# Performance work log

Measured on AMD Instinct MI355X. Metric: run time of the kernel, lower is better.

## Reference

```python
import jax, jax.numpy as jnp
import numpy as np

ALPHA = 1.0


def setup_inputs() -> dict:
    key = jax.random.key(0)
    k1, k2 = jax.random.split(key)
    B, T, N, L = 512, 50, 6400, 10
    spikes = jax.random.uniform(k1, (B, T, N), dtype=jnp.float32)
    labels = jax.random.randint(k2, (B,), 0, L, dtype=jnp.int64)
    rates = jnp.zeros((N, L), dtype=jnp.float32)
    return {"spikes": spikes, "labels": labels, "rates": rates, "n_labels": L}


def reference(spikes, labels, rates, n_labels):
    # spikes: [B, T, N]; labels: [B]; rates: [N, L]
    s = spikes.sum(axis=1)  # [B, N] spike counts per sample
    # segment-sum over batch keyed by label (replaces per-label nonzero+gather loop)
    seg_sum = jax.ops.segment_sum(s, labels, num_segments=n_labels)          # [L, N]
    counts = jax.ops.segment_sum(jnp.ones(labels.shape, s.dtype), labels,
                                 num_segments=n_labels)                       # [L]
    mean = seg_sum / jnp.maximum(counts, 1.0)[:, None]                        # [L, N]
    # original only updates column i when that label is present in the batch
    rates_new = jnp.where(counts[None, :] > 0, ALPHA * rates + mean.T, rates)  # [N, L]
    assignments = jnp.argmax(rates_new, axis=1)                               # [N]
    return assignments, rates_new
```

## Files before the change

### kernel.cpp

```cpp
#include <hip/hip_runtime.h>
#include <math.h>


#define L_FIXED 10

__global__ void __launch_bounds__(64) partial2_k(
    const float* __restrict__ spikes, const int* __restrict__ labels,
    float* __restrict__ part, int B, int T, int N, int GB) {
    const int g = blockIdx.y;
    const int v = blockIdx.x * blockDim.x + threadIdx.x;
    const int V = N >> 1;
    if (v >= V) return;

    float a0[L_FIXED], a1[L_FIXED];
#pragma unroll
    for (int l = 0; l < L_FIXED; ++l) { a0[l] = 0.f; a1[l] = 0.f; }

    const int b0 = g * GB;
    const int b1 = (b0 + GB < B) ? (b0 + GB) : B;
    for (int b = b0; b < b1; ++b) {
        const float2* p = (const float2*)(spikes + (size_t)b * T * N) + v;
        float s0 = 0.f, s1 = 0.f;
#pragma unroll 10
        for (int t = 0; t < T; ++t) {
            float2 x = p[(size_t)t * V];
            s0 += x.x; s1 += x.y;
        }
        const int lab = labels[b];
#pragma unroll
        for (int l = 0; l < L_FIXED; ++l)
            if (lab == l) { a0[l] += s0; a1[l] += s1; }
    }

    float* dst = part + (size_t)g * L_FIXED * N;
#pragma unroll
    for (int l = 0; l < L_FIXED; ++l) {
        ((float2*)(dst + (size_t)l * N))[v] = make_float2(a0[l], a1[l]);
    }
}

__global__ void __launch_bounds__(64) partial1_k(
    const float* __restrict__ spikes, const int* __restrict__ labels,
    float* __restrict__ part, int B, int T, int N, int GB) {
    const int g = blockIdx.y;
    const int n = blockIdx.x * blockDim.x + threadIdx.x;
    if (n >= N) return;

    float a[L_FIXED];
#pragma unroll
    for (int l = 0; l < L_FIXED; ++l) a[l] = 0.f;

    const int b0 = g * GB;
    const int b1 = (b0 + GB < B) ? (b0 + GB) : B;
    for (int b = b0; b < b1; ++b) {
        const float* p = spikes + (size_t)b * T * N + n;
        float s = 0.f;
#pragma unroll 10
        for (int t = 0; t < T; ++t) s += p[(size_t)t * N];
        const int lab = labels[b];
#pragma unroll
        for (int l = 0; l < L_FIXED; ++l)
            if (lab == l) a[l] += s;
    }
    float* dst = part + (size_t)g * L_FIXED * N;
#pragma unroll
    for (int l = 0; l < L_FIXED; ++l) dst[(size_t)l * N + n] = a[l];
}

__global__ void __launch_bounds__(256) finalize_k(
    const float* __restrict__ part, const int* __restrict__ labels,
    const float* __restrict__ rates, float* __restrict__ out,
    int B, int N, int NG, float alpha) {
    __shared__ int cnt[L_FIXED];
    if (threadIdx.x < L_FIXED) cnt[threadIdx.x] = 0;
    __syncthreads();
    for (int b = threadIdx.x; b < B; b += blockDim.x)
        atomicAdd(&cnt[labels[b]], 1);
    __syncthreads();

    const int n = blockIdx.x * blockDim.x + threadIdx.x;
    if (n >= N) return;

    float best = -INFINITY;
    int bi = 0;
#pragma unroll
    for (int l = 0; l < L_FIXED; ++l) {
        double s = 0.0;
        for (int g = 0; g < NG; ++g)
            s += (double)part[((size_t)g * L_FIXED + l) * N + n];
        const int c = cnt[l];
        const float r = rates[(size_t)n * L_FIXED + l];
        const float v = (c > 0) ? (alpha * r + (float)(s / (double)c)) : r;
        out[(size_t)N + (size_t)n * L_FIXED + l] = v;
        if (v > best) { best = v; bi = l; }
    }
    out[n] = (float)bi;
}

extern "C" void kernel_launch(void* const* d_in, const int* in_sizes, int n_in,
                              void* d_out, int out_size, void* d_ws, size_t ws_size,
                              hipStream_t stream) {
    const float* spikes = (const float*)d_in[0];
    const int*   labels = (const int*)d_in[1];
    const float* rates  = (const float*)d_in[2];
    const int L = L_FIXED;
    const int B = in_sizes[1];
    const int N = in_sizes[2] / L;
    const int T = in_sizes[0] / (B * N);
    float* out = (float*)d_out;

    const size_t per = (size_t)L * N * sizeof(float);
    int NG = 64;
    if (per > 0 && (size_t)NG * per > ws_size) NG = (int)(ws_size / per);
    if (NG < 1) NG = 1;
    if (NG > B) NG = B;
    const int GB = (B + NG - 1) / NG;
    float* part = (float*)d_ws;

    if ((N & 1) == 0) {
        const int V = N >> 1;
        dim3 g((V + 63) / 64, NG);
        partial2_k<<<g, dim3(64), 0, stream>>>(spikes, labels, part, B, T, N, GB);
    } else {
        dim3 g((N + 63) / 64, NG);
        partial1_k<<<g, dim3(64), 0, stream>>>(spikes, labels, part, B, T, N, GB);
    }

    finalize_k<<<dim3((N + 255) / 256), dim3(256), 0, stream>>>(
        part, labels, rates, out, B, N, NG, 1.0f);
}
```

Baseline: 987.9 us.

## Split time-sum per sample and move label bucketing into a parallel finalize

The first stage now launches one block per (sample, time-half) and sums spikes over time with float4 loads into a per-sample partial buffer, instead of grouping batches per thread with per-label accumulators. The finalize kernel then does the label segment-sum itself, splitting partial rows across 8 wavefronts with labels cached in shared memory, and reduces those in shared memory before applying the rate update and argmax. The aim is higher occupancy and wider contiguous loads in the bandwidth-bound reduction. The cost is a larger intermediate buffer (HS*B*N floats) that finalize must read back, which adds memory traffic.

```diff
diff --git a/kernel.cpp b/kernel.cpp
--- a/kernel.cpp
+++ b/kernel.cpp
@@ -4,98 +4,127 @@
 
 #define L_FIXED 10
 
-__global__ void __launch_bounds__(64) partial2_k(
-    const float* __restrict__ spikes, const int* __restrict__ labels,
-    float* __restrict__ part, int B, int T, int N, int GB) {
-    const int g = blockIdx.y;
-    const int v = blockIdx.x * blockDim.x + threadIdx.x;
-    const int V = N >> 1;
-    if (v >= V) return;
+__global__ void __launch_bounds__(320) sumT_lin_k(
+    const float* __restrict__ spikes, float* __restrict__ part,
+    int B, int T, int N, int HS) {
+    const int r = blockIdx.x;
+    const int h = r / B;
+    const int b = r - h * B;
+    const int t0 = (T * h) / HS;
+    const int t1 = (T * (h + 1)) / HS;
+    const int V = N >> 2;
+    const int tid = threadIdx.x;
+    const float4* p = (const float4*)(spikes + (size_t)b * T * N);
+    float4* dst = (float4*)(part + (size_t)r * N);
 
-    float a0[L_FIXED], a1[L_FIXED];
-#pragma unroll
-    for (int l = 0; l < L_FIXED; ++l) { a0[l] = 0.f; a1[l] = 0.f; }
-
-    const int b0 = g * GB;
-    const int b1 = (b0 + GB < B) ? (b0 + GB) : B;
-    for (int b = b0; b < b1; ++b) {
-        const float2* p = (const float2*)(spikes + (size_t)b * T * N) + v;
-        float s0 = 0.f, s1 = 0.f;
-#pragma unroll 10
-        for (int t = 0; t < T; ++t) {
-            float2 x = p[(size_t)t * V];
-            s0 += x.x; s1 += x.y;
+    for (int v0 = 0; v0 < V; v0 += 1600) {
+        float4 a0 = make_float4(0.f, 0.f, 0.f, 0.f);
+        float4 a1 = a0, a2 = a0, a3 = a0, a4 = a0;
+        const int c0 = v0 + tid;
+#pragma unroll 2
+        for (int t = t0; t < t1; ++t) {
+            const float4* row = p + (size_t)t * V;
+            if (c0 < V)        { float4 x = row[c0];        a0.x += x.x; a0.y += x.y; a0.z += x.z; a0.w += x.w; }
+            if (c0 + 320 < V)  { float4 x = row[c0 + 320];  a1.x += x.x; a1.y += x.y; a1.z += x.z; a1.w += x.w; }
+            if (c0 + 640 < V)  { float4 x = row[c0 + 640];  a2.x += x.x; a2.y += x.y; a2.z += x.z; a2.w += x.w; }
+            if (c0 + 960 < V)  { float4 x = row[c0 + 960];  a3.x += x.x; a3.y += x.y; a3.z += x.z; a3.w += x.w; }
+            if (c0 + 1280 < V) { float4 x = row[c0 + 1280]; a4.x += x.x; a4.y += x.y; a4.z += x.z; a4.w += x.w; }
         }
-        const int lab = labels[b];
-#pragma unroll
-        for (int l = 0; l < L_FIXED; ++l)
-            if (lab == l) { a0[l] += s0; a1[l] += s1; }
-    }
-
-    float* dst = part + (size_t)g * L_FIXED * N;
-#pragma unroll
-    for (int l = 0; l < L_FIXED; ++l) {
-        ((float2*)(dst + (size_t)l * N))[v] = make_float2(a0[l], a1[l]);
+        if (c0 < V)        dst[c0]        = a0;
+        if (c0 + 320 < V)  dst[c0 + 320]  = a1;
+        if (c0 + 640 < V)  dst[c0 + 640]  = a2;
+        if (c0 + 960 < V)  dst[c0 + 960]  = a3;
+        if (c0 + 1280 < V) dst[c0 + 1280] = a4;
     }
 }
 
-__global__ void __launch_bounds__(64) partial1_k(
-    const float* __restrict__ spikes, const int* __restrict__ labels,
-    float* __restrict__ part, int B, int T, int N, int GB) {
-    const int g = blockIdx.y;
+__global__ void __launch_bounds__(256) sumT1h_k(
+    const float* __restrict__ spikes, float* __restrict__ part,
+    int B, int T, int N, int HS) {
+    const int r = blockIdx.y;
+    const int h = r / B;
+    const int b = r - h * B;
+    const int t0 = (T * h) / HS;
+    const int t1 = (T * (h + 1)) / HS;
     const int n = blockIdx.x * blockDim.x + threadIdx.x;
     if (n >= N) return;
-
-    float a[L_FIXED];
-#pragma unroll
-    for (int l = 0; l < L_FIXED; ++l) a[l] = 0.f;
-
-    const int b0 = g * GB;
-    const int b1 = (b0 + GB < B) ? (b0 + GB) : B;
-    for (int b = b0; b < b1; ++b) {
-        const float* p = spikes + (size_t)b * T * N + n;
-        float s = 0.f;
-#pragma unroll 10
-        for (int t = 0; t < T; ++t) s += p[(size_t)t * N];
-        const int lab = labels[b];
-#pragma unroll
-        for (int l = 0; l < L_FIXED; ++l)
-            if (lab == l) a[l] += s;
-    }
-    float* dst = part + (size_t)g * L_FIXED * N;
-#pragma unroll
-    for (int l = 0; l < L_FIXED; ++l) dst[(size_t)l * N + n] = a[l];
+    const float* p = spikes + (size_t)b * T * N + n;
+    float s = 0.f;
+    for (int t = t0; t < t1; ++t) s += p[(size_t)t * N];
+    part[(size_t)r * N + n] = s;
 }
 
-__global__ void __launch_bounds__(256) finalize_k(
+__global__ void __launch_bounds__(512) finalize2_k(
     const float* __restrict__ part, const int* __restrict__ labels,
     const float* __restrict__ rates, float* __restrict__ out,
-    int B, int N, int NG, float alpha) {
+    int B, int N, int NR, float alpha) {
     __shared__ int cnt[L_FIXED];
-    if (threadIdx.x < L_FIXED) cnt[threadIdx.x] = 0;
+    __shared__ short slab[2048];
+    __shared__ double red[8][64][L_FIXED];
+
+    const int tid = threadIdx.x;
+    if (tid < L_FIXED) cnt[tid] = 0;
     __syncthreads();
-    for (int b = threadIdx.x; b < B; b += blockDim.x)
-        atomicAdd(&cnt[labels[b]], 1);
+    const bool use_slab = (NR <= 2048);
+    const int HS = NR / B;
+    for (int i = tid; i < B; i += blockDim.x) {
+        const int lb = labels[i];
+        atomicAdd(&cnt[lb], 1);
+        if (use_slab)
+            for (int h = 0; h < HS; ++h) slab[h * B + i] = (short)lb;
+    }
     __syncthreads();
 
-    const int n = blockIdx.x * blockDim.x + threadIdx.x;
-    if (n >= N) return;
+    const int lane = tid & 63;
+    const int q = tid >> 6;
+    const int n = blockIdx.x * 64 + lane;
 
-    float best = -INFINITY;
-    int bi = 0;
+    double a[L_FIXED];
 #pragma unroll
-    for (int l = 0; l < L_FIXED; ++l) {
-        double s = 0.0;
-        for (int g = 0; g < NG; ++g)
-            s += (double)part[((size_t)g * L_FIXED + l) * N + n];
-        const int c = cnt[l];
-        const float r = rates[(size_t)n * L_FIXED + l];
-        const float v = (c > 0) ? (alpha * r + (float)(s / (double)c)) : r;
-        out[(size_t)N + (size_t)n * L_FIXED + l] = v;
-        if (v > best) { best = v; bi = l; }
+    for (int l = 0; l < L_FIXED; ++l) a[l] = 0.0;
+
+    if (n < N) {
+        if (use_slab) {
+#pragma unroll 4
+            for (int r = q; r < NR; r += 8) {
+                const float s = part[(size_t)r * N + n];
+                const int lab = slab[r];
+#pragma unroll
+                for (int l = 0; l < L_FIXED; ++l)
+                    if (lab == l) a[l] += (double)s;
+            }
+        } else {
+            for (int r = q; r < NR; r += 8) {
+                const float s = part[(size_t)r * N + n];
+                const int lab = labels[r % B];
+#pragma unroll
+                for (int l = 0; l < L_FIXED; ++l)
+                    if (lab == l) a[l] += (double)s;
+            }
+        }
     }
-    out[n] = (float)bi;
+#pragma unroll
+    for (int l = 0; l < L_FIXED; ++l) red[q][lane][l] = a[l];
+    __syncthreads();
+
+    if (q == 0 && n < N) {
+        float best = -INFINITY;
+        int bi = 0;
+#pragma unroll
+        for (int l = 0; l < L_FIXED; ++l) {
+            double s = 0.0;
+#pragma unroll
+            for (int qq = 0; qq < 8; ++qq) s += red[qq][lane][l];
+            const int c = cnt[l];
+            const float r0 = rates[(size_t)n * L_FIXED + l];
+            const float v = (c > 0) ? (alpha * r0 + (float)(s / (double)c)) : r0;
+            out[(size_t)N + (size_t)n * L_FIXED + l] = v;
+            if (v > best) { best = v; bi = l; }
+        }
+        out[n] = (float)bi;
+    }
 }
+
 
 extern "C" void kernel_launch(void* const* d_in, const int* in_sizes, int n_in,
                               void* d_out, int out_size, void* d_ws, size_t ws_size,
@@ -108,24 +137,19 @@
     const int N = in_sizes[2] / L;
     const int T = in_sizes[0] / (B * N);
     float* out = (float*)d_out;
-
-    const size_t per = (size_t)L * N * sizeof(float);
-    int NG = 64;
-    if (per > 0 && (size_t)NG * per > ws_size) NG = (int)(ws_size / per);
-    if (NG < 1) NG = 1;
-    if (NG > B) NG = B;
-    const int GB = (B + NG - 1) / NG;
     float* part = (float*)d_ws;
 
-    if ((N & 1) == 0) {
-        const int V = N >> 1;
-        dim3 g((V + 63) / 64, NG);
-        partial2_k<<<g, dim3(64), 0, stream>>>(spikes, labels, part, B, T, N, GB);
+    int HS = (T >= 2) ? 2 : 1;
+    if ((size_t)HS * B * N * sizeof(float) > ws_size) HS = 1;
+    const int NR = HS * B;
+
+    if ((N & 3) == 0) {
+        sumT_lin_k<<<dim3(NR), dim3(320), 0, stream>>>(spikes, part, B, T, N, HS);
     } else {
-        dim3 g((N + 63) / 64, NG);
-        partial1_k<<<g, dim3(64), 0, stream>>>(spikes, labels, part, B, T, N, GB);
+        dim3 g((N + 255) / 256, NR);
+        sumT1h_k<<<g, dim3(256), 0, stream>>>(spikes, part, B, T, N, HS);
     }
 
-    finalize_k<<<dim3((N + 255) / 256), dim3(256), 0, stream>>>(
-        part, labels, rates, out, B, N, NG, 1.0f);
+    finalize2_k<<<dim3((N + 63) / 64), dim3(512), 0, stream>>>(
+        part, labels, rates, out, B, N, NR, 1.0f);
 }
```

Measured after the change: 852.2 us. -13.7%, faster.
